# Kernel optimization log

Hardware: AMD Instinct MI355X
Metric: run time of the kernel (lower is better)

## Reference

```python
import jax, jax.numpy as jnp
import numpy as np


def setup_inputs() -> dict:
    key = jax.random.key(0)
    k1, k2 = jax.random.split(key)
    # positive inputs -> positive matmul outputs, so log is well-defined
    x = jax.random.uniform(k1, (8, 2048, 1024), dtype=jnp.float32)
    matrix = jax.random.uniform(k2, (1024, 1024), dtype=jnp.float32)
    return {"x": x, "matrix": matrix}


def reference(x, matrix):
    # mm_big: shifted quantized matmul; mm_small: no-shift quantized matmul.
    # In float math both compute the same product (quantization differs only
    # in fixed-point scaling), so we compute it once; XLA would CSE anyway.
    y_big = jnp.einsum('bsk,km->bsm', x, matrix)    # [B,S,M]
    y_small = jnp.einsum('bsk,km->bsm', x, matrix)  # NoShiftMM, same float math

    big = (y_big > 0).astype(x.dtype)   # gt0
    small = 1.0 - big                   # oplus(neg(big)) = 1 + (-big)

    eps = jnp.finfo(x.dtype).tiny
    # AddIdentityTLUT(torch.log): LUT approximation of log; float reference is log.
    z_big = jnp.log(jnp.maximum(y_big, eps)) * big      # lut_big -> mul_big
    z_small = jnp.log(jnp.maximum(y_small, eps)) * small  # lut_small -> mul_small
    return z_big + z_small  # add_output
```

## Files before the change

kernel.cpp:

```cpp
#include <hip/hip_runtime.h>
#include <cstdint>
#include <cstddef>

#define M_GLOB 16384
#define N_GLOB 1024
#define K_GLOB 1024

#define BM 128
#define BN 128
#define BKF 128

typedef unsigned char  u8;
typedef unsigned short u16;
typedef __attribute__((ext_vector_type(4))) float  f32x4;
typedef __attribute__((ext_vector_type(16))) float f32x16;
typedef __attribute__((ext_vector_type(4))) unsigned int  u32x4;
typedef __attribute__((ext_vector_type(2))) unsigned int  u32x2;
typedef __attribute__((ext_vector_type(8))) int  i32x8;
typedef __attribute__((ext_vector_type(8))) __bf16 bf16x8;

static __device__ __forceinline__ unsigned pack2_bf16(float lo, float hi) {
    unsigned bl = __builtin_bit_cast(unsigned, lo);
    unsigned bh = __builtin_bit_cast(unsigned, hi);
    return (bh & 0xFFFF0000u) | (bl >> 16);
}

static __device__ __forceinline__ unsigned cvt4_fp8(float a, float b, float c, float d) {
    int w = __builtin_amdgcn_cvt_pk_fp8_f32(a, b, 0, false);
    w = __builtin_amdgcn_cvt_pk_fp8_f32(c, d, w, true);
    return (unsigned)w;
}

static __device__ __forceinline__ void gload_lds16(const u8* g, char* l) {
    __builtin_amdgcn_global_load_lds(
        (const __attribute__((address_space(1))) unsigned int*)g,
        (__attribute__((address_space(3))) unsigned int*)l,
        16, 0, 0);
}

__global__ __launch_bounds__(256)
void prep_fp8_kernel(const float* __restrict__ A, u8* __restrict__ Ab,
                     const float* __restrict__ B, u8* __restrict__ Bt, int nA) {
    __shared__ float tile[32][33];
    const int tid = threadIdx.x;
    if ((int)blockIdx.x < nA) {
        const size_t i = ((size_t)blockIdx.x * 256 + tid) * 16;
        f32x4 f0 = *(const f32x4*)(A + i);
        f32x4 f1 = *(const f32x4*)(A + i + 4);
        f32x4 f2 = *(const f32x4*)(A + i + 8);
        f32x4 f3 = *(const f32x4*)(A + i + 12);
        u32x4 o;
        o.x = cvt4_fp8(f0.x, f0.y, f0.z, f0.w);
        o.y = cvt4_fp8(f1.x, f1.y, f1.z, f1.w);
        o.z = cvt4_fp8(f2.x, f2.y, f2.z, f2.w);
        o.w = cvt4_fp8(f3.x, f3.y, f3.z, f3.w);
        *(u32x4*)(Ab + i) = o;
    } else {
        const int bid = (int)blockIdx.x - nA;
        const int n0 = (bid & 31) * 32;
        const int k0 = (bid >> 5) * 32;
        const int tx = tid & 31;
        const int ty = tid >> 5;
#pragma unroll
        for (int i = 0; i < 32; i += 8)
            tile[ty + i][tx] = B[(size_t)(k0 + ty + i) * N_GLOB + n0 + tx];
        __syncthreads();
#pragma unroll
        for (int i = 0; i < 32; i += 8) {
            int w = __builtin_amdgcn_cvt_pk_fp8_f32(tile[tx][ty + i], 0.f, 0, false);
            Bt[(size_t)(n0 + ty + i) * K_GLOB + k0 + tx] = (u8)(w & 0xFF);
        }
    }
}

__global__ __launch_bounds__(256, 3)
void gemm_mx_kernel(const u8* __restrict__ A,
                    const u8* __restrict__ Bt,
                    float* __restrict__ C)
{
    __shared__ __attribute__((aligned(16))) char smem[32768];
    float* Cs = (float*)smem;

    const int tid  = threadIdx.x;
    const int wave = tid >> 6;
    const int lane = tid & 63;
    const int wr   = wave >> 1;
    const int wc   = wave & 1;
    const int l32  = lane & 31;
    const int half = lane >> 5;

    const int b    = (int)blockIdx.x;
    const int xcd  = b & 7;
    const int idx  = b >> 3;
    const int m0   = (xcd * 16 + (idx >> 3)) * BM;
    const int n0   = (idx & 7) * BN;

    const int srow = lane >> 3;
    const int sp   = lane & 7;
    const int sc   = sp ^ srow;
    const u8* gA = A  + (size_t)(m0 + srow) * K_GLOB + sc * 16;
    const u8* gB = Bt + (size_t)(n0 + srow) * K_GLOB + sc * 16;
    char* ldsA = smem + wave * 1024;
    char* ldsB = smem + 16384 + wave * 1024;

    f32x16 acc[2][2];
#pragma unroll
    for (int i = 0; i < 2; ++i)
#pragma unroll
        for (int j = 0; j < 2; ++j)
#pragma unroll
            for (int r = 0; r < 16; ++r)
                acc[i][j][r] = 0.f;

    const int swz = lane & 7;
    const int scale1 = 0x7F7F7F7F;

    for (int kt = 0; kt < K_GLOB / BKF; ++kt) {
        const int ko = kt * BKF;
#pragma unroll
        for (int s = 0; s < 4; ++s)
            gload_lds16(gA + (size_t)(s * 4 + wave) * 8 * K_GLOB + ko,
                        ldsA + s * 4096);
#pragma unroll
        for (int s = 0; s < 4; ++s)
            gload_lds16(gB + (size_t)(s * 4 + wave) * 8 * K_GLOB + ko,
                        ldsB + s * 4096);
        __syncthreads();

#pragma unroll
        for (int s = 0; s < 2; ++s) {
            const int c0 = s * 4 + half * 2;
            const int p0 = ((c0    ) ^ swz) * 16;
            const int p1 = ((c0 + 1) ^ swz) * 16;
            i32x8 af[2], bf[2];
#pragma unroll
            for (int i = 0; i < 2; ++i) {
                const int row = wr * 64 + i * 32 + l32;
                u32x4 lo = *(const u32x4*)(smem + row * 128 + p0);
                u32x4 hi = *(const u32x4*)(smem + row * 128 + p1);
                af[i][0] = lo.x; af[i][1] = lo.y; af[i][2] = lo.z; af[i][3] = lo.w;
                af[i][4] = hi.x; af[i][5] = hi.y; af[i][6] = hi.z; af[i][7] = hi.w;
            }
#pragma unroll
            for (int j = 0; j < 2; ++j) {
                const int row = wc * 64 + j * 32 + l32;
                u32x4 lo = *(const u32x4*)(smem + 16384 + row * 128 + p0);
                u32x4 hi = *(const u32x4*)(smem + 16384 + row * 128 + p1);
                bf[j][0] = lo.x; bf[j][1] = lo.y; bf[j][2] = lo.z; bf[j][3] = lo.w;
                bf[j][4] = hi.x; bf[j][5] = hi.y; bf[j][6] = hi.z; bf[j][7] = hi.w;
            }
#pragma unroll
            for (int i = 0; i < 2; ++i)
#pragma unroll
                for (int j = 0; j < 2; ++j)
                    acc[i][j] = __builtin_amdgcn_mfma_scale_f32_32x32x64_f8f6f4(
                        af[i], bf[j], acc[i][j],
                        0 , 0 ,
                        0, scale1, 0, scale1);
        }
        __syncthreads();
    }

    const float LN2 = 0.69314718055994530942f;
    const int c4 = tid & 31;
    const int r0 = tid >> 5;
#pragma unroll
    for (int h = 0; h < 4; ++h) {
        __syncthreads();
        if (wr == (h >> 1)) {
            const int i = h & 1;
#pragma unroll
            for (int j = 0; j < 2; ++j) {
                const int col = wc * 64 + j * 32 + l32;
#pragma unroll
                for (int r = 0; r < 16; ++r) {
                    const int row32 = (r & 3) + 8 * (r >> 2) + 4 * half;
                    float v = fmaxf(acc[i][j][r], 1.17549435e-38f);
                    Cs[row32 * 132 + col] = __log2f(v) * LN2;
                }
            }
        }
        __syncthreads();
#pragma unroll
        for (int s2 = 0; s2 < 4; ++s2) {
            const int row = s2 * 8 + r0;
            f32x4 v = *(const f32x4*)&Cs[row * 132 + c4 * 4];
            __builtin_nontemporal_store(v,
                (f32x4*)&C[(size_t)(m0 + h * 32 + row) * N_GLOB + n0 + c4 * 4]);
        }
    }
}

#define FBM 128
#define FBN 128
#define LDK 40
__global__ __launch_bounds__(256)
void logmm_fused_kernel(const float* __restrict__ A,
                        const float* __restrict__ Bf,
                        float* __restrict__ C)
{
    __shared__ u16 As[FBM][LDK];
    __shared__ u16 Bs[FBN][LDK];

    const int tid  = threadIdx.x;
    const int lane = tid & 63;
    const int wave = tid >> 6;
    const int wr   = wave >> 1;
    const int wc   = wave & 1;
    const int quad = lane >> 4;
    const int l16  = lane & 15;

    const int m0 = blockIdx.y * FBM;
    const int n0 = blockIdx.x * FBN;

    f32x4 acc[4][4];
#pragma unroll
    for (int i = 0; i < 4; ++i)
#pragma unroll
        for (int j = 0; j < 4; ++j)
            acc[i][j] = f32x4{0.f, 0.f, 0.f, 0.f};

    const int ga_row = tid >> 2;
    const int ga_c8  = (tid & 3) * 8;
    const int fb_nt = tid >> 3;
    const int fb_kt = tid & 7;

    for (int kt = 0; kt < K_GLOB / 32; ++kt) {
        const int k0 = kt * 32;
#pragma unroll
        for (int s = 0; s < 2; ++s) {
            const int row = ga_row + s * 64;
            const float* src = A + (size_t)(m0 + row) * K_GLOB + k0 + ga_c8;
            f32x4 f0 = *(const f32x4*)src;
            f32x4 f1 = *(const f32x4*)(src + 4);
            u32x4 o;
            o.x = pack2_bf16(f0.x, f0.y);
            o.y = pack2_bf16(f0.z, f0.w);
            o.z = pack2_bf16(f1.x, f1.y);
            o.w = pack2_bf16(f1.z, f1.w);
            *(u32x4*)&As[row][ga_c8] = o;
        }
        {
            f32x4 r0 = *(const f32x4*)(Bf + (size_t)(k0 + fb_kt * 4 + 0) * N_GLOB + n0 + fb_nt * 4);
            f32x4 r1 = *(const f32x4*)(Bf + (size_t)(k0 + fb_kt * 4 + 1) * N_GLOB + n0 + fb_nt * 4);
            f32x4 r2 = *(const f32x4*)(Bf + (size_t)(k0 + fb_kt * 4 + 2) * N_GLOB + n0 + fb_nt * 4);
            f32x4 r3 = *(const f32x4*)(Bf + (size_t)(k0 + fb_kt * 4 + 3) * N_GLOB + n0 + fb_nt * 4);
#pragma unroll
            for (int j = 0; j < 4; ++j) {
                u32x2 o;
                o.x = pack2_bf16(r0[j], r1[j]);
                o.y = pack2_bf16(r2[j], r3[j]);
                *(u32x2*)&Bs[fb_nt * 4 + j][fb_kt * 4] = o;
            }
        }

        __syncthreads();

        bf16x8 af[4], bfr[4];
#pragma unroll
        for (int i = 0; i < 4; ++i)
            af[i] = __builtin_bit_cast(bf16x8, *(const u32x4*)&As[wr * 64 + i * 16 + l16][quad * 8]);
#pragma unroll
        for (int j = 0; j < 4; ++j)
            bfr[j] = __builtin_bit_cast(bf16x8, *(const u32x4*)&Bs[wc * 64 + j * 16 + l16][quad * 8]);

#pragma unroll
        for (int i = 0; i < 4; ++i)
#pragma unroll
            for (int j = 0; j < 4; ++j)
                acc[i][j] = __builtin_amdgcn_mfma_f32_16x16x32_bf16(af[i], bfr[j], acc[i][j], 0, 0, 0);

        __syncthreads();
    }

    const float LN2 = 0.69314718055994530942f;
#pragma unroll
    for (int i = 0; i < 4; ++i) {
#pragma unroll
        for (int j = 0; j < 4; ++j) {
            const int col = n0 + wc * 64 + j * 16 + l16;
#pragma unroll
            for (int r = 0; r < 4; ++r) {
                const int row = m0 + wr * 64 + i * 16 + quad * 4 + r;
                float v = fmaxf(acc[i][j][r], 1.17549435e-38f);
                C[(size_t)row * N_GLOB + col] = __log2f(v) * LN2;
            }
        }
    }
}

extern "C" void kernel_launch(void* const* d_in, const int* in_sizes, int n_in,
                              void* d_out, int out_size, void* d_ws, size_t ws_size,
                              hipStream_t stream) {
    const float* A = (const float*)d_in[0];
    const float* B = (const float*)d_in[1];
    float* C = (float*)d_out;

    const size_t bt_bytes = (size_t)N_GLOB * K_GLOB;
    const size_t ab_bytes = (size_t)M_GLOB * K_GLOB;
    const int nA = (M_GLOB * K_GLOB) / (256 * 16);

    if (ws_size >= bt_bytes + ab_bytes) {
        u8* Bt = (u8*)d_ws;
        u8* Ab = (u8*)d_ws + bt_bytes;
        prep_fp8_kernel<<<nA + 1024, 256, 0, stream>>>(A, Ab, B, Bt, nA);
        gemm_mx_kernel<<<(M_GLOB / BM) * (N_GLOB / BN), 256, 0, stream>>>(Ab, Bt, C);
    } else {
        logmm_fused_kernel<<<dim3(N_GLOB / FBN, M_GLOB / FBM), 256, 0, stream>>>(A, B, C);
    }
}
```

Measured before the change: 132.5 us.

## Fuse A fp8 quantization into GEMM with LDS-resident A strip and double-buffered B

Removes the separate pass that quantizes A to fp8 in global memory. Each block now converts a 64-row strip of A straight into LDS (64 KB) and reuses it across all four 256-column chunks of N, while B tiles are double-buffered with async global-to-LDS loads and manual vmcnt waits. This cuts the A-side global write and read traffic, but uses 128 KB of LDS per block, so only one block fits per CU. The grid shrinks to 256 blocks, and the epilogue writes scalar non-temporal stores instead of going through LDS for coalescing.

```diff
diff --git a/kernel.cpp b/kernel.cpp
--- a/kernel.cpp
+++ b/kernel.cpp
@@ -6,9 +6,11 @@
 #define N_GLOB 1024
 #define K_GLOB 1024
 
-#define BM 128
-#define BN 128
-#define BKF 128
+#define BM   64
+#define BNC  256
+#define NCH  4
+#define NKT  8
+#define NT   32
 
 typedef unsigned char  u8;
 typedef unsigned short u16;
@@ -31,6 +33,12 @@
     return (unsigned)w;
 }
 
+static __device__ __forceinline__ void barrier_raw() {
+    asm volatile("s_barrier" ::: "memory");
+}
+
+#define VMCNT(n) asm volatile("s_waitcnt vmcnt(" #n ")" ::: "memory")
+
 static __device__ __forceinline__ void gload_lds16(const u8* g, char* l) {
     __builtin_amdgcn_global_load_lds(
         (const __attribute__((address_space(1))) unsigned int*)g,
@@ -39,47 +47,31 @@
 }
 
 __global__ __launch_bounds__(256)
-void prep_fp8_kernel(const float* __restrict__ A, u8* __restrict__ Ab,
-                     const float* __restrict__ B, u8* __restrict__ Bt, int nA) {
+void prep_b_kernel(const float* __restrict__ B, u8* __restrict__ Bt) {
     __shared__ float tile[32][33];
     const int tid = threadIdx.x;
-    if ((int)blockIdx.x < nA) {
-        const size_t i = ((size_t)blockIdx.x * 256 + tid) * 16;
-        f32x4 f0 = *(const f32x4*)(A + i);
-        f32x4 f1 = *(const f32x4*)(A + i + 4);
-        f32x4 f2 = *(const f32x4*)(A + i + 8);
-        f32x4 f3 = *(const f32x4*)(A + i + 12);
-        u32x4 o;
-        o.x = cvt4_fp8(f0.x, f0.y, f0.z, f0.w);
-        o.y = cvt4_fp8(f1.x, f1.y, f1.z, f1.w);
-        o.z = cvt4_fp8(f2.x, f2.y, f2.z, f2.w);
-        o.w = cvt4_fp8(f3.x, f3.y, f3.z, f3.w);
-        *(u32x4*)(Ab + i) = o;
-    } else {
-        const int bid = (int)blockIdx.x - nA;
-        const int n0 = (bid & 31) * 32;
-        const int k0 = (bid >> 5) * 32;
-        const int tx = tid & 31;
-        const int ty = tid >> 5;
-#pragma unroll
-        for (int i = 0; i < 32; i += 8)
-            tile[ty + i][tx] = B[(size_t)(k0 + ty + i) * N_GLOB + n0 + tx];
-        __syncthreads();
-#pragma unroll
-        for (int i = 0; i < 32; i += 8) {
-            int w = __builtin_amdgcn_cvt_pk_fp8_f32(tile[tx][ty + i], 0.f, 0, false);
-            Bt[(size_t)(n0 + ty + i) * K_GLOB + k0 + tx] = (u8)(w & 0xFF);
-        }
-    }
-}
-
-__global__ __launch_bounds__(256, 3)
-void gemm_mx_kernel(const u8* __restrict__ A,
-                    const u8* __restrict__ Bt,
-                    float* __restrict__ C)
+    const int bid = (int)blockIdx.x;
+    const int n0 = (bid & 31) * 32;
+    const int k0 = (bid >> 5) * 32;
+    const int tx = tid & 31;
+    const int ty = tid >> 5;
+#pragma unroll
+    for (int i = 0; i < 32; i += 8)
+        tile[ty + i][tx] = B[(size_t)(k0 + ty + i) * N_GLOB + n0 + tx];
+    __syncthreads();
+#pragma unroll
+    for (int i = 0; i < 32; i += 8) {
+        int w = __builtin_amdgcn_cvt_pk_fp8_f32(tile[tx][ty + i], 0.f, 0, false);
+        Bt[(size_t)(n0 + ty + i) * K_GLOB + k0 + tx] = (u8)(w & 0xFF);
+    }
+}
+
+__global__ __launch_bounds__(256)
+void gemm_fused_lds_kernel(const float* __restrict__ A,
+                           const u8* __restrict__ Bt,
+                           float* __restrict__ C)
 {
-    __shared__ __attribute__((aligned(16))) char smem[32768];
-    float* Cs = (float*)smem;
+    __shared__ __attribute__((aligned(16))) char smem[131072];
 
     const int tid  = threadIdx.x;
     const int wave = tid >> 6;
@@ -88,107 +80,126 @@
     const int wc   = wave & 1;
     const int l32  = lane & 31;
     const int half = lane >> 5;
-
-    const int b    = (int)blockIdx.x;
-    const int xcd  = b & 7;
-    const int idx  = b >> 3;
-    const int m0   = (xcd * 16 + (idx >> 3)) * BM;
-    const int n0   = (idx & 7) * BN;
+    const int swz  = lane & 7;
+
+    const int b   = (int)blockIdx.x;
+    const int m0  = b * BM;
+    const int ch0 = (b >> 3) & 3;
 
     const int srow = lane >> 3;
     const int sp   = lane & 7;
     const int sc   = sp ^ srow;
-    const u8* gA = A  + (size_t)(m0 + srow) * K_GLOB + sc * 16;
-    const u8* gB = Bt + (size_t)(n0 + srow) * K_GLOB + sc * 16;
-    char* ldsA = smem + wave * 1024;
-    char* ldsB = smem + 16384 + wave * 1024;
-
-    f32x16 acc[2][2];
-#pragma unroll
-    for (int i = 0; i < 2; ++i)
-#pragma unroll
-        for (int j = 0; j < 2; ++j)
+
+    const int scale1 = 0x7F7F7F7F;
+    const float LN2 = 0.69314718055994530942f;
+
+#define STAGE(v, bufsel)                                                      \
+    {                                                                         \
+        const int chv = (((v) >> 3) + ch0) & 3;                               \
+        const int ktv = (v) & 7;                                              \
+        const u8* srcb = Bt + (size_t)(chv * BNC + srow) * K_GLOB             \
+                            + ktv * 128 + sc * 16;                            \
+        char* dstb = smem + 65536 + (bufsel) * 32768 + wave * 1024;           \
+        _Pragma("unroll")                                                     \
+        for (int s_ = 0; s_ < 8; ++s_)                                        \
+            gload_lds16(srcb + (size_t)(s_ * 4 + wave) * 8 * K_GLOB,         \
+                        dstb + s_ * 4096);                                    \
+    }
+
+    STAGE(0, 0);
+
+    {
+        const int cpos = tid & 63;
+#pragma unroll 4
+        for (int p = 0; p < 16; ++p) {
+            const int row = p * 4 + wave;
+            const float* src = A + (size_t)(m0 + row) * K_GLOB + cpos * 16;
+            f32x4 f0 = *(const f32x4*)(src);
+            f32x4 f1 = *(const f32x4*)(src + 4);
+            f32x4 f2 = *(const f32x4*)(src + 8);
+            f32x4 f3 = *(const f32x4*)(src + 12);
+            u32x4 o;
+            o.x = cvt4_fp8(f0.x, f0.y, f0.z, f0.w);
+            o.y = cvt4_fp8(f1.x, f1.y, f1.z, f1.w);
+            o.z = cvt4_fp8(f2.x, f2.y, f2.z, f2.w);
+            o.w = cvt4_fp8(f3.x, f3.y, f3.z, f3.w);
+            const int pos = cpos ^ (row & 7);
+            *(u32x4*)(smem + row * 1024 + pos * 16) = o;
+        }
+    }
+    __syncthreads();
+
+    const char* aBase = smem + (size_t)(wr * 32 + l32) * 1024;
+
+    for (int cc = 0; cc < NCH; ++cc) {
+        const int ch  = (cc + ch0) & 3;
+        const int n0c = ch * BNC;
+
+        f32x16 acc[4];
+#pragma unroll
+        for (int j = 0; j < 4; ++j)
 #pragma unroll
             for (int r = 0; r < 16; ++r)
-                acc[i][j][r] = 0.f;
-
-    const int swz = lane & 7;
-    const int scale1 = 0x7F7F7F7F;
-
-    for (int kt = 0; kt < K_GLOB / BKF; ++kt) {
-        const int ko = kt * BKF;
-#pragma unroll
-        for (int s = 0; s < 4; ++s)
-            gload_lds16(gA + (size_t)(s * 4 + wave) * 8 * K_GLOB + ko,
-                        ldsA + s * 4096);
-#pragma unroll
-        for (int s = 0; s < 4; ++s)
-            gload_lds16(gB + (size_t)(s * 4 + wave) * 8 * K_GLOB + ko,
-                        ldsB + s * 4096);
-        __syncthreads();
-
-#pragma unroll
-        for (int s = 0; s < 2; ++s) {
-            const int c0 = s * 4 + half * 2;
-            const int p0 = ((c0    ) ^ swz) * 16;
-            const int p1 = ((c0 + 1) ^ swz) * 16;
-            i32x8 af[2], bf[2];
-#pragma unroll
-            for (int i = 0; i < 2; ++i) {
-                const int row = wr * 64 + i * 32 + l32;
-                u32x4 lo = *(const u32x4*)(smem + row * 128 + p0);
-                u32x4 hi = *(const u32x4*)(smem + row * 128 + p1);
-                af[i][0] = lo.x; af[i][1] = lo.y; af[i][2] = lo.z; af[i][3] = lo.w;
-                af[i][4] = hi.x; af[i][5] = hi.y; af[i][6] = hi.z; af[i][7] = hi.w;
-            }
-#pragma unroll
-            for (int j = 0; j < 2; ++j) {
-                const int row = wc * 64 + j * 32 + l32;
-                u32x4 lo = *(const u32x4*)(smem + 16384 + row * 128 + p0);
-                u32x4 hi = *(const u32x4*)(smem + 16384 + row * 128 + p1);
-                bf[j][0] = lo.x; bf[j][1] = lo.y; bf[j][2] = lo.z; bf[j][3] = lo.w;
-                bf[j][4] = hi.x; bf[j][5] = hi.y; bf[j][6] = hi.z; bf[j][7] = hi.w;
-            }
-#pragma unroll
-            for (int i = 0; i < 2; ++i)
-#pragma unroll
-                for (int j = 0; j < 2; ++j)
-                    acc[i][j] = __builtin_amdgcn_mfma_scale_f32_32x32x64_f8f6f4(
-                        af[i], bf[j], acc[i][j],
+                acc[j][r] = 0.f;
+
+        for (int kt = 0; kt < NKT; ++kt) {
+            const int v = cc * NKT + kt;
+            if (v + 1 < NT) {
+                STAGE(v + 1, (v + 1) & 1);
+                VMCNT(8);
+            } else {
+                VMCNT(0);
+            }
+            barrier_raw();
+
+            const char* bBase = smem + 65536 + (v & 1) * 32768;
+#pragma unroll
+            for (int s = 0; s < 2; ++s) {
+                const int c0l = s * 4 + half * 2;
+                const int p0 = ((c0l    ) ^ swz) * 16;
+                const int p1 = ((c0l + 1) ^ swz) * 16;
+                i32x8 af;
+                {
+                    u32x4 lo = *(const u32x4*)(aBase + kt * 128 + p0);
+                    u32x4 hi = *(const u32x4*)(aBase + kt * 128 + p1);
+                    af[0] = lo.x; af[1] = lo.y; af[2] = lo.z; af[3] = lo.w;
+                    af[4] = hi.x; af[5] = hi.y; af[6] = hi.z; af[7] = hi.w;
+                }
+                i32x8 bf[4];
+#pragma unroll
+                for (int j = 0; j < 4; ++j) {
+                    const char* bRow = bBase + (size_t)(wc * 128 + j * 32 + l32) * 128;
+                    u32x4 lo = *(const u32x4*)(bRow + p0);
+                    u32x4 hi = *(const u32x4*)(bRow + p1);
+                    bf[j][0] = lo.x; bf[j][1] = lo.y; bf[j][2] = lo.z; bf[j][3] = lo.w;
+                    bf[j][4] = hi.x; bf[j][5] = hi.y; bf[j][6] = hi.z; bf[j][7] = hi.w;
+                }
+#pragma unroll
+                for (int j = 0; j < 4; ++j)
+                    acc[j] = __builtin_amdgcn_mfma_scale_f32_32x32x64_f8f6f4(
+                        af, bf[j], acc[j],
                         0 , 0 ,
                         0, scale1, 0, scale1);
-        }
-        __syncthreads();
-    }
-
-    const float LN2 = 0.69314718055994530942f;
-    const int c4 = tid & 31;
-    const int r0 = tid >> 5;
-#pragma unroll
-    for (int h = 0; h < 4; ++h) {
-        __syncthreads();
-        if (wr == (h >> 1)) {
-            const int i = h & 1;
-#pragma unroll
-            for (int j = 0; j < 2; ++j) {
-                const int col = wc * 64 + j * 32 + l32;
+            }
+            barrier_raw();
+        }
+
+        {
+            const int rowBase = m0 + wr * 32 + 4 * half;
+#pragma unroll
+            for (int j = 0; j < 4; ++j) {
+                const int col = n0c + wc * 128 + j * 32 + l32;
 #pragma unroll
                 for (int r = 0; r < 16; ++r) {
-                    const int row32 = (r & 3) + 8 * (r >> 2) + 4 * half;
-                    float v = fmaxf(acc[i][j][r], 1.17549435e-38f);
-                    Cs[row32 * 132 + col] = __log2f(v) * LN2;
+                    const int row = rowBase + (r & 3) + 8 * (r >> 2);
+                    float vv = fmaxf(acc[j][r], 1.17549435e-38f);
+                    __builtin_nontemporal_store(__log2f(vv) * LN2,
+                        &C[(size_t)row * N_GLOB + col]);
                 }
             }
         }
-        __syncthreads();
-#pragma unroll
-        for (int s2 = 0; s2 < 4; ++s2) {
-            const int row = s2 * 8 + r0;
-            f32x4 v = *(const f32x4*)&Cs[row * 132 + c4 * 4];
-            __builtin_nontemporal_store(v,
-                (f32x4*)&C[(size_t)(m0 + h * 32 + row) * N_GLOB + n0 + c4 * 4]);
-        }
-    }
+    }
+#undef STAGE
 }
 
 #define FBM 128
@@ -297,14 +308,11 @@
     float* C = (float*)d_out;
 
     const size_t bt_bytes = (size_t)N_GLOB * K_GLOB;
-    const size_t ab_bytes = (size_t)M_GLOB * K_GLOB;
-    const int nA = (M_GLOB * K_GLOB) / (256 * 16);
-
-    if (ws_size >= bt_bytes + ab_bytes) {
+
+    if (ws_size >= bt_bytes) {
         u8* Bt = (u8*)d_ws;
-        u8* Ab = (u8*)d_ws + bt_bytes;
-        prep_fp8_kernel<<<nA + 1024, 256, 0, stream>>>(A, Ab, B, Bt, nA);
-        gemm_mx_kernel<<<(M_GLOB / BM) * (N_GLOB / BN), 256, 0, stream>>>(Ab, Bt, C);
+        prep_b_kernel<<<1024, 256, 0, stream>>>(B, Bt);
+        gemm_fused_lds_kernel<<<M_GLOB / BM, 256, 0, stream>>>(A, Bt, C);
     } else {
         logmm_fused_kernel<<<dim3(N_GLOB / FBN, M_GLOB / FBM), 256, 0, stream>>>(A, B, C);
     }
```

Measured after the change: 218.7 us. 1.65x slower.

## Register-prefetch GEMM tiles and process two N-tiles per block sequentially

Applied to the files above, without the earlier changes.

Replaces direct global-to-LDS loads with register-staged prefetch: the next k-tile is loaded into registers while MFMAs run on the current LDS tile. Each block now computes two consecutive 128-column output tiles, which halves the grid and reuses the A rows from L2, with the log epilogue run after each tile. Occupancy drops from 3 to 2 blocks per CU, and a raw s_barrier replaces the trailing syncthreads. This trades more register pressure and fewer resident blocks for better latency hiding of the global loads.

```diff
diff --git a/kernel.cpp b/kernel.cpp
--- a/kernel.cpp
+++ b/kernel.cpp
@@ -31,11 +31,8 @@
     return (unsigned)w;
 }
 
-static __device__ __forceinline__ void gload_lds16(const u8* g, char* l) {
-    __builtin_amdgcn_global_load_lds(
-        (const __attribute__((address_space(1))) unsigned int*)g,
-        (__attribute__((address_space(3))) unsigned int*)l,
-        16, 0, 0);
+static __device__ __forceinline__ void barrier_raw() {
+    asm volatile("s_barrier" ::: "memory");
 }
 
 __global__ __launch_bounds__(256)
@@ -73,12 +70,12 @@
     }
 }
 
-__global__ __launch_bounds__(256, 3)
+__global__ __launch_bounds__(256, 2)
 void gemm_mx_kernel(const u8* __restrict__ A,
                     const u8* __restrict__ Bt,
                     float* __restrict__ C)
 {
-    __shared__ __attribute__((aligned(16))) char smem[32768];
+    __shared__ __attribute__((aligned(16))) char smem[33792];
     float* Cs = (float*)smem;
 
     const int tid  = threadIdx.x;
@@ -89,19 +86,17 @@
     const int l32  = lane & 31;
     const int half = lane >> 5;
 
-    const int b    = (int)blockIdx.x;
-    const int xcd  = b & 7;
-    const int idx  = b >> 3;
-    const int m0   = (xcd * 16 + (idx >> 3)) * BM;
-    const int n0   = (idx & 7) * BN;
+    const int b     = (int)blockIdx.x;
+    const int xcd   = b & 7;
+    const int i2    = b >> 3;
+    const int m0    = (xcd * 16 + (i2 >> 2)) * BM;
+    const int nbase = (i2 & 3) * 256;
 
     const int srow = lane >> 3;
     const int sp   = lane & 7;
     const int sc   = sp ^ srow;
-    const u8* gA = A  + (size_t)(m0 + srow) * K_GLOB + sc * 16;
-    const u8* gB = Bt + (size_t)(n0 + srow) * K_GLOB + sc * 16;
-    char* ldsA = smem + wave * 1024;
-    char* ldsB = smem + 16384 + wave * 1024;
+    const u8* gA  = A  + (size_t)(m0 + srow) * K_GLOB + sc * 16;
+    const u8* gB0 = Bt + (size_t)(nbase + srow) * K_GLOB + sc * 16;
 
     f32x16 acc[2][2];
 #pragma unroll
@@ -114,18 +109,37 @@
 
     const int swz = lane & 7;
     const int scale1 = 0x7F7F7F7F;
-
-    for (int kt = 0; kt < K_GLOB / BKF; ++kt) {
-        const int ko = kt * BKF;
-#pragma unroll
-        for (int s = 0; s < 4; ++s)
-            gload_lds16(gA + (size_t)(s * 4 + wave) * 8 * K_GLOB + ko,
-                        ldsA + s * 4096);
-#pragma unroll
-        for (int s = 0; s < 4; ++s)
-            gload_lds16(gB + (size_t)(s * 4 + wave) * 8 * K_GLOB + ko,
-                        ldsB + s * 4096);
+    const float LN2 = 0.69314718055994530942f;
+    const int c4 = tid & 31;
+    const int r0 = tid >> 5;
+
+    u32x4 ra[4], rb[4];
+#pragma unroll
+    for (int s = 0; s < 4; ++s) {
+        ra[s] = *(const u32x4*)(gA  + (size_t)((s * 4 + wave) * 8) * K_GLOB);
+        rb[s] = *(const u32x4*)(gB0 + (size_t)((s * 4 + wave) * 8) * K_GLOB);
+    }
+
+    for (int v = 0; v < 16; ++v) {
+#pragma unroll
+        for (int s = 0; s < 4; ++s) {
+            const int row = (s * 4 + wave) * 8 + srow;
+            *(u32x4*)(smem + row * 128 + sp * 16) = ra[s];
+            *(u32x4*)(smem + 16384 + row * 128 + sp * 16) = rb[s];
+        }
         __syncthreads();
+
+        if (v + 1 < 16) {
+            const int ktn = (v + 1) & 7;
+            const int chn = (v + 1) >> 3;
+            const u8* gBn = gB0 + (size_t)(chn * BN) * K_GLOB + ktn * BKF;
+            const u8* gAn = gA + ktn * BKF;
+#pragma unroll
+            for (int s = 0; s < 4; ++s) {
+                ra[s] = *(const u32x4*)(gAn + (size_t)((s * 4 + wave) * 8) * K_GLOB);
+                rb[s] = *(const u32x4*)(gBn + (size_t)((s * 4 + wave) * 8) * K_GLOB);
+            }
+        }
 
 #pragma unroll
         for (int s = 0; s < 2; ++s) {
@@ -158,35 +172,47 @@
                         0 , 0 ,
                         0, scale1, 0, scale1);
         }
-        __syncthreads();
-    }
-
-    const float LN2 = 0.69314718055994530942f;
-    const int c4 = tid & 31;
-    const int r0 = tid >> 5;
-#pragma unroll
-    for (int h = 0; h < 4; ++h) {
-        __syncthreads();
-        if (wr == (h >> 1)) {
-            const int i = h & 1;
-#pragma unroll
-            for (int j = 0; j < 2; ++j) {
-                const int col = wc * 64 + j * 32 + l32;
-#pragma unroll
-                for (int r = 0; r < 16; ++r) {
-                    const int row32 = (r & 3) + 8 * (r >> 2) + 4 * half;
-                    float v = fmaxf(acc[i][j][r], 1.17549435e-38f);
-                    Cs[row32 * 132 + col] = __log2f(v) * LN2;
+        barrier_raw();
+
+        if ((v & 7) == 7) {
+            const int n0c = nbase + (v >> 3) * BN;
+#pragma unroll
+            for (int h = 0; h < 2; ++h) {
+                __syncthreads();
+                if (wr == h) {
+#pragma unroll
+                    for (int i = 0; i < 2; ++i) {
+#pragma unroll
+                        for (int j = 0; j < 2; ++j) {
+                            const int col = wc * 64 + j * 32 + l32;
+#pragma unroll
+                            for (int r = 0; r < 16; ++r) {
+                                const int row32 = (r & 3) + 8 * (r >> 2) + 4 * half;
+                                float vv = fmaxf(acc[i][j][r], 1.17549435e-38f);
+                                Cs[(i * 32 + row32) * 132 + col] = __log2f(vv) * LN2;
+                            }
+                        }
+                    }
                 }
-            }
-        }
-        __syncthreads();
-#pragma unroll
-        for (int s2 = 0; s2 < 4; ++s2) {
-            const int row = s2 * 8 + r0;
-            f32x4 v = *(const f32x4*)&Cs[row * 132 + c4 * 4];
-            __builtin_nontemporal_store(v,
-                (f32x4*)&C[(size_t)(m0 + h * 32 + row) * N_GLOB + n0 + c4 * 4]);
+                __syncthreads();
+#pragma unroll
+                for (int s2 = 0; s2 < 8; ++s2) {
+                    const int row = s2 * 8 + r0;
+                    f32x4 vv = *(const f32x4*)&Cs[row * 132 + c4 * 4];
+                    __builtin_nontemporal_store(vv,
+                        (f32x4*)&C[(size_t)(m0 + h * 64 + row) * N_GLOB + n0c + c4 * 4]);
+                }
+            }
+            __syncthreads();
+            if (v == 7) {
+#pragma unroll
+                for (int i = 0; i < 2; ++i)
+#pragma unroll
+                    for (int j = 0; j < 2; ++j)
+#pragma unroll
+                        for (int r = 0; r < 16; ++r)
+                            acc[i][j][r] = 0.f;
+            }
         }
     }
 }
@@ -304,7 +330,7 @@
         u8* Bt = (u8*)d_ws;
         u8* Ab = (u8*)d_ws + bt_bytes;
         prep_fp8_kernel<<<nA + 1024, 256, 0, stream>>>(A, Ab, B, Bt, nA);
-        gemm_mx_kernel<<<(M_GLOB / BM) * (N_GLOB / BN), 256, 0, stream>>>(Ab, Bt, C);
+        gemm_mx_kernel<<<(M_GLOB / BM) * (N_GLOB / 256), 256, 0, stream>>>(Ab, Bt, C);
     } else {
         logmm_fused_kernel<<<dim3(N_GLOB / FBN, M_GLOB / FBM), 256, 0, stream>>>(A, B, C);
     }
```

New measurement: 134.4 us. No clear change (+1.4%).
